# Optimization experiments

Measured on AMD Instinct MI355X. Metric: run time of the kernel, lower is better.

Reference implementation:

```python
import jax, jax.numpy as jnp
import numpy as np

B, L, H, HD, NK, NQ = 2, 1024, 2048, 64, 4, 32
NPREV = NQ - NK  # 28 KV heads gathered from previous layers


def _rotate_half(x):
    x1, x2 = jnp.split(x, 2, axis=-1)
    return jnp.concatenate((-x2, x1), axis=-1)


def _apply_rope(cos, sin, x):
    length = x.shape[-2]
    return x * cos[..., -length:, :] + _rotate_half(x) * sin[..., -length:, :]


def setup_inputs() -> dict:
    key = jax.random.key(0)
    ks = jax.random.split(key, 7)
    hidden_states = jax.random.normal(ks[0], (B, L, H), jnp.float32)
    prev_k = jax.random.normal(ks[1], (B, NPREV, L, HD), jnp.float32)
    prev_v = jax.random.normal(ks[2], (B, NPREV, L, HD), jnp.float32)
    s = 0.02
    Wq = jax.random.normal(ks[3], (NQ * HD, H), jnp.float32) * s
    Wk = jax.random.normal(ks[4], (NK * HD, H), jnp.float32) * s
    Wv = jax.random.normal(ks[5], (NK * HD, H), jnp.float32) * s
    Wo = jax.random.normal(ks[6], (H, NQ * HD), jnp.float32) * s
    # RoPE tables (duplicated-half layout matching rotate_half)
    inv_freq = 1.0 / (10000.0 ** (jnp.arange(0, HD, 2, dtype=jnp.float32) / HD))
    freqs = jnp.arange(L, dtype=jnp.float32)[:, None] * inv_freq[None, :]
    emb = jnp.concatenate((freqs, freqs), axis=-1)  # [L, HD]
    cos = jnp.cos(emb)[None, None]  # [1,1,L,HD]
    sin = jnp.sin(emb)[None, None]
    attention_mask = jnp.tril(jnp.ones((L, L), dtype=bool))[None, None]  # [1,1,L,L]
    return {"hidden_states": hidden_states, "prev_k": prev_k, "prev_v": prev_v,
            "Wq": Wq, "Wk": Wk, "Wv": Wv, "Wo": Wo,
            "cos": cos, "sin": sin, "attention_mask": attention_mask}


def reference(hidden_states, prev_k, prev_v, Wq, Wk, Wv, Wo, cos, sin, attention_mask):
    Bv, Lv, _ = hidden_states.shape
    # QKV projections (torch Linear: x @ W.T)
    q = (hidden_states @ Wq.T).reshape(Bv, Lv, NQ, HD).transpose(0, 2, 1, 3)  # [B,NQ,L,HD]
    k_new = (hidden_states @ Wk.T).reshape(Bv, Lv, NK, HD).transpose(0, 2, 1, 3)
    v_new = (hidden_states @ Wv.T).reshape(Bv, Lv, NK, HD).transpose(0, 2, 1, 3)
    # DeCAN cross-layer cache update: stack previous layers' KV heads + current
    k = jnp.concatenate((prev_k, k_new), axis=1)  # [B,NQ,L,HD]
    v = jnp.concatenate((prev_v, v_new), axis=1)
    # RoPE after cache gather (same positions for all stacked layers)
    q = _apply_rope(cos, sin, q)
    k = _apply_rope(cos, sin, k)
    # SDPA with additive log-mask (log(bool) == 0 / -inf; broadcast == repeat)
    add_mask = jnp.where(attention_mask, jnp.float32(0.0), jnp.float32(-1e30))
    scores = jnp.einsum('bhqd,bhkd->bhqk', q, k) * (HD ** -0.5) + add_mask
    attn = jax.nn.softmax(scores, axis=-1)
    out = jnp.einsum('bhqk,bhkd->bhqd', attn, v)  # [B,NQ,L,HD]
    out = out.transpose(0, 2, 1, 3).reshape(Bv, Lv, NQ * HD)
    return out @ Wo.T  # [B,L,H]
```

## Files before the change

kernel.cpp:

```cpp
#include <hip/hip_runtime.h>
#include <stdint.h>

#define L_SEQ 1024
#define NHEAD 32
#define NPREV 28
#define HDIM  64
#define HID   2048
#define NPROJ 2560

typedef __bf16 bf16_t;
typedef bf16_t bf16x8 __attribute__((ext_vector_type(8)));
typedef float  f32x4  __attribute__((ext_vector_type(4)));

__device__ __forceinline__ ushort f2bf(float x) {
    union { float f; uint32_t u; } v; v.f = x;
    uint32_t r = v.u + 0x7fffu + ((v.u >> 16) & 1u);
    return (ushort)(r >> 16);
}
__device__ __forceinline__ ushort f2bf_t(float x) {
    union { float f; uint32_t u; } v; v.f = x;
    return (ushort)(v.u >> 16);
}
__device__ __forceinline__ float bf2f(ushort u) {
    union { uint32_t u; float f; } v; v.u = ((uint32_t)u) << 16; return v.f;
}
__device__ __forceinline__ void cvt8(float* dst, uint4 u) {
    union { uint32_t u; float f; } t;
    t.u = u.x << 16;         dst[0] = t.f;
    t.u = u.x & 0xffff0000u; dst[1] = t.f;
    t.u = u.y << 16;         dst[2] = t.f;
    t.u = u.y & 0xffff0000u; dst[3] = t.f;
    t.u = u.z << 16;         dst[4] = t.f;
    t.u = u.z & 0xffff0000u; dst[5] = t.f;
    t.u = u.w << 16;         dst[6] = t.f;
    t.u = u.w & 0xffff0000u; dst[7] = t.f;
}

#define GLB(p) ((const __attribute__((address_space(1))) void*)(p))
#define LDS(p) ((__attribute__((address_space(3))) void*)(p))

__global__ void cvt_all(const float* __restrict__ s0, const float* __restrict__ s1,
                        const float* __restrict__ s2, const float* __restrict__ s3,
                        const float* __restrict__ s4,
                        ushort* __restrict__ d0, ushort* __restrict__ d1,
                        ushort* __restrict__ d2, ushort* __restrict__ d3,
                        ushort* __restrict__ d4) {
    int blk = blockIdx.x;
    const float* src; ushort* dst; int idx;
    if      (blk < 4096) { src = s0; dst = d0; idx = blk; }
    else if (blk < 8192) { src = s1; dst = d1; idx = blk - 4096; }
    else if (blk < 8704) { src = s2; dst = d2; idx = blk - 8192; }
    else if (blk < 9216) { src = s3; dst = d3; idx = blk - 8704; }
    else                 { src = s4; dst = d4; idx = blk - 9216; }
    int i = idx * 256 + threadIdx.x;
    float4 v = ((const float4*)src)[i];
    ushort4 o;
    o.x = f2bf(v.x); o.y = f2bf(v.y); o.z = f2bf(v.z); o.w = f2bf(v.w);
    ((ushort4*)dst)[i] = o;
}

__global__ __launch_bounds__(256, 3) void gemm1_fused(
        const ushort* __restrict__ A, const ushort* __restrict__ B,
        ushort* __restrict__ C0, ushort* __restrict__ C1,
        const float* __restrict__ prev_k, const float* __restrict__ prev_v,
        const float* __restrict__ cosb, const float* __restrict__ sinb,
        ushort* __restrict__ Kr, ushort* __restrict__ Vt) {
    __shared__ __align__(16) ushort Ash[2 * 4096];
    __shared__ __align__(16) ushort Bsh[2 * 8192];
    const int g   = blockIdx.x;
    const int tid = threadIdx.x;

    if (g < 1280) {
        const int K = 2048, N = NPROJ;
        const int lane = tid & 63;
        const int wave = tid >> 6;
        const int quad = lane >> 4;
        const int l16  = lane & 15;
        const int z  = g / 640;
        const int rb = g % 640;
        const int n0 = (rb % 20) * 128;
        const int m0 = (rb / 20) * 64;
        const int wm = (wave >> 1) * 32;
        const int wn = (wave & 1) * 64;
        const int kb = z * 1024;
        const int ke = kb + 1024;
        ushort* C = z ? C1 : C0;

        f32x4 acc[2][4] = {};

        const int sb = ((tid & 3) ^ ((tid >> 3) & 3)) * 8;
        const ushort* Ag = A + (long)(m0 + (tid >> 2)) * K + sb;
        const ushort* Bg = B + (long)(n0 + (tid >> 2)) * K + sb;
        const int woff = wave * 512;
        const int swz = (quad ^ ((l16 >> 1) & 3)) * 8;

        __builtin_amdgcn_global_load_lds(GLB(Ag + kb),                LDS(Ash + woff),               16, 0, 0);
        __builtin_amdgcn_global_load_lds(GLB(Ag + kb + 32),           LDS(Ash + 2048 + woff),        16, 0, 0);
        __builtin_amdgcn_global_load_lds(GLB(Bg + kb),                LDS(Bsh + woff),               16, 0, 0);
        __builtin_amdgcn_global_load_lds(GLB(Bg + 64L * K + kb),      LDS(Bsh + 2048 + woff),        16, 0, 0);
        __builtin_amdgcn_global_load_lds(GLB(Bg + kb + 32),           LDS(Bsh + 4096 + woff),        16, 0, 0);
        __builtin_amdgcn_global_load_lds(GLB(Bg + 64L * K + kb + 32), LDS(Bsh + 4096 + 2048 + woff), 16, 0, 0);

        int cur = 0;
        for (int k0 = kb; k0 < ke; k0 += 64) {
            __syncthreads();
            if (k0 + 64 < ke) {
                const int na = (cur ^ 1) * 4096;
                const int nb = (cur ^ 1) * 8192;
                const ushort* Agn = Ag + k0 + 64;
                const ushort* Bgn = Bg + k0 + 64;
                __builtin_amdgcn_global_load_lds(GLB(Agn),                LDS(Ash + na + woff),               16, 0, 0);
                __builtin_amdgcn_global_load_lds(GLB(Agn + 32),           LDS(Ash + na + 2048 + woff),        16, 0, 0);
                __builtin_amdgcn_global_load_lds(GLB(Bgn),                LDS(Bsh + nb + woff),               16, 0, 0);
                __builtin_amdgcn_global_load_lds(GLB(Bgn + 64L * K),      LDS(Bsh + nb + 2048 + woff),        16, 0, 0);
                __builtin_amdgcn_global_load_lds(GLB(Bgn + 32),           LDS(Bsh + nb + 4096 + woff),        16, 0, 0);
                __builtin_amdgcn_global_load_lds(GLB(Bgn + 64L * K + 32), LDS(Bsh + nb + 4096 + 2048 + woff), 16, 0, 0);
            }
            const ushort* As = Ash + cur * 4096;
            const ushort* Bs = Bsh + cur * 8192;
#pragma unroll
            for (int h = 0; h < 2; h++) {
                bf16x8 af[2], bf[4];
#pragma unroll
                for (int i = 0; i < 2; i++)
                    af[i] = *(const bf16x8*)(As + h * 2048 + (wm + i * 16 + l16) * 32 + swz);
#pragma unroll
                for (int i = 0; i < 4; i++)
                    bf[i] = *(const bf16x8*)(Bs + h * 4096 + (wn + i * 16 + l16) * 32 + swz);
#pragma unroll
                for (int mi = 0; mi < 2; mi++)
#pragma unroll
                    for (int ni = 0; ni < 4; ni++)
                        acc[mi][ni] = __builtin_amdgcn_mfma_f32_16x16x32_bf16(af[mi], bf[ni], acc[mi][ni], 0, 0, 0);
            }
            cur ^= 1;
        }
#pragma unroll
        for (int mi = 0; mi < 2; mi++)
#pragma unroll
            for (int ni = 0; ni < 4; ni++)
#pragma unroll
                for (int r = 0; r < 4; r++) {
                    int m = m0 + wm + mi * 16 + quad * 4 + r;
                    int n = n0 + wn + ni * 16 + l16;
                    C[(long)m * N + n] = f2bf(acc[mi][ni][r]);
                }
    } else {
        const int idx = g - 1280;
        const int lt  = idx & 15;
        const int ph  = idx >> 4;
        const int b   = ph / NPREV;
        const int h   = ph % NPREV;
        const int l0  = lt * 64;
        const int r   = tid >> 2;
        const int c0  = (tid & 3) * 8;
        const int l   = l0 + r;
        const int bh  = b * NHEAD + h;
        const long base = (long)bh * (L_SEQ * HDIM);

        float cv[8], sv[8];
        *(float4*)(cv)     = *(const float4*)(cosb + l * 64 + c0);
        *(float4*)(cv + 4) = *(const float4*)(cosb + l * 64 + c0 + 4);
        *(float4*)(sv)     = *(const float4*)(sinb + l * 64 + c0);
        *(float4*)(sv + 4) = *(const float4*)(sinb + l * 64 + c0 + 4);

        {
            const float* pk = prev_k + (((long)b * NPREV + h) * L_SEQ + l) * 64;
            float xl[8], xh[8];
            *(float4*)(xl)     = *(const float4*)(pk + c0);
            *(float4*)(xl + 4) = *(const float4*)(pk + c0 + 4);
            *(float4*)(xh)     = *(const float4*)(pk + c0 + 32);
            *(float4*)(xh + 4) = *(const float4*)(pk + c0 + 36);
            ushort ol[8], oh[8];
#pragma unroll
            for (int i = 0; i < 8; i++) {
                ol[i] = f2bf(xl[i] * cv[i] - xh[i] * sv[i]);
                oh[i] = f2bf(xh[i] * cv[i] + xl[i] * sv[i]);
            }
            ushort* k = Kr + base + (long)l * 64;
            *(uint4*)(k + c0)      = *(uint4*)ol;
            *(uint4*)(k + c0 + 32) = *(uint4*)oh;
        }
        {
            ushort* T = Ash;
            const float* pv = prev_v + (((long)b * NPREV + h) * L_SEQ + l) * 64;
            float xl[8], xh[8];
            *(float4*)(xl)     = *(const float4*)(pv + c0);
            *(float4*)(xl + 4) = *(const float4*)(pv + c0 + 4);
            *(float4*)(xh)     = *(const float4*)(pv + c0 + 32);
            *(float4*)(xh + 4) = *(const float4*)(pv + c0 + 36);
#pragma unroll
            for (int i = 0; i < 8; i++) {
                T[(c0 + i) * 72 + r]      = f2bf(xl[i]);
                T[(c0 + 32 + i) * 72 + r] = f2bf(xh[i]);
            }
            __syncthreads();
            const int lc = (tid & 3) * 16;
            uint4 o0 = *(const uint4*)(T + r * 72 + lc);
            uint4 o1 = *(const uint4*)(T + r * 72 + lc + 8);
            ushort* og = Vt + base + (long)r * L_SEQ + l0 + lc;
            *(uint4*)og       = o0;
            *(uint4*)(og + 8) = o1;
        }
    }
}

__global__ __launch_bounds__(256) void prep_new(const ushort* __restrict__ pa,
                                                const ushort* __restrict__ pb,
                                                const float* __restrict__ cosb,
                                                const float* __restrict__ sinb,
                                                ushort* __restrict__ Qr,
                                                ushort* __restrict__ Kr,
                                                ushort* __restrict__ Vt) {
    __shared__ __align__(16) ushort T[64 * 72];
    const int t  = threadIdx.x;
    const int l0 = blockIdx.x * 64;
    const int bh = blockIdx.y;
    const int b  = bh >> 5, h = bh & 31;
    const int r  = t >> 2;
    const int c0 = (t & 3) * 8;
    const int l  = l0 + r;
    const long prow = ((long)(b * L_SEQ + l)) * NPROJ;
    const long base = (long)bh * (L_SEQ * HDIM);

    float cv[8], sv[8];
    *(float4*)(cv)     = *(const float4*)(cosb + l * 64 + c0);
    *(float4*)(cv + 4) = *(const float4*)(cosb + l * 64 + c0 + 4);
    *(float4*)(sv)     = *(const float4*)(sinb + l * 64 + c0);
    *(float4*)(sv + 4) = *(const float4*)(sinb + l * 64 + c0 + 4);

    const float SC = 0.125f * 1.44269504f;

    {
        float xl[8], xh[8], yl[8], yh[8];
        cvt8(xl, *(const uint4*)(pa + prow + h * 64 + c0));
        cvt8(xh, *(const uint4*)(pa + prow + h * 64 + c0 + 32));
        cvt8(yl, *(const uint4*)(pb + prow + h * 64 + c0));
        cvt8(yh, *(const uint4*)(pb + prow + h * 64 + c0 + 32));
        ushort ol[8], oh[8];
#pragma unroll
        for (int i = 0; i < 8; i++) {
            float a = xl[i] + yl[i], c = xh[i] + yh[i];
            ol[i] = f2bf((a * cv[i] - c * sv[i]) * SC);
            oh[i] = f2bf((c * cv[i] + a * sv[i]) * SC);
        }
        ushort* q = Qr + base + (long)l * 64;
        *(uint4*)(q + c0)      = *(uint4*)ol;
        *(uint4*)(q + c0 + 32) = *(uint4*)oh;
    }
    if (h < NPREV) return;

    {
        float xl[8], xh[8], yl[8], yh[8];
        cvt8(xl, *(const uint4*)(pa + prow + HID + (h - NPREV) * 64 + c0));
        cvt8(xh, *(const uint4*)(pa + prow + HID + (h - NPREV) * 64 + c0 + 32));
        cvt8(yl, *(const uint4*)(pb + prow + HID + (h - NPREV) * 64 + c0));
        cvt8(yh, *(const uint4*)(pb + prow + HID + (h - NPREV) * 64 + c0 + 32));
        ushort ol[8], oh[8];
#pragma unroll
        for (int i = 0; i < 8; i++) {
            float a = xl[i] + yl[i], c = xh[i] + yh[i];
            ol[i] = f2bf(a * cv[i] - c * sv[i]);
            oh[i] = f2bf(c * cv[i] + a * sv[i]);
        }
        ushort* k = Kr + base + (long)l * 64;
        *(uint4*)(k + c0)      = *(uint4*)ol;
        *(uint4*)(k + c0 + 32) = *(uint4*)oh;
    }
    {
        float xl[8], xh[8], yl[8], yh[8];
        cvt8(xl, *(const uint4*)(pa + prow + HID + 256 + (h - NPREV) * 64 + c0));
        cvt8(xh, *(const uint4*)(pa + prow + HID + 256 + (h - NPREV) * 64 + c0 + 32));
        cvt8(yl, *(const uint4*)(pb + prow + HID + 256 + (h - NPREV) * 64 + c0));
        cvt8(yh, *(const uint4*)(pb + prow + HID + 256 + (h - NPREV) * 64 + c0 + 32));
#pragma unroll
        for (int i = 0; i < 8; i++) {
            T[(c0 + i) * 72 + r]      = f2bf(xl[i] + yl[i]);
            T[(c0 + 32 + i) * 72 + r] = f2bf(xh[i] + yh[i]);
        }
        __syncthreads();
        const int lc = (t & 3) * 16;
        uint4 o0 = *(const uint4*)(T + r * 72 + lc);
        uint4 o1 = *(const uint4*)(T + r * 72 + lc + 8);
        ushort* og = Vt + base + (long)r * L_SEQ + l0 + lc;
        *(uint4*)og       = o0;
        *(uint4*)(og + 8) = o1;
    }
}

#define KP 68
__global__ __launch_bounds__(256, 4) void attn_mfma(const ushort* __restrict__ Qr,
                                                    const ushort* __restrict__ Kr,
                                                    const ushort* __restrict__ Vt,
                                                    ushort* __restrict__ Oa) {
    __shared__ __align__(16) ushort Ksh[64 * KP];
    __shared__ __align__(16) ushort Vsh[64 * KP];
    __shared__ __align__(16) ushort Psh[4][16 * KP];

    const int tid  = threadIdx.x;
    const int lane = tid & 63;
    const int wave = tid >> 6;
    const int quad = lane >> 4;
    const int l16  = lane & 15;
    const int bh   = blockIdx.x;
    const int q0   = (15 - (int)blockIdx.y) * 64;
    const long base = (long)bh * (L_SEQ * HDIM);

    bf16x8 qf0, qf1;
    {
        const ushort* qp = Qr + base + (long)(q0 + wave * 16 + l16) * HDIM + quad * 8;
        qf0 = *(const bf16x8*)qp;
        qf1 = *(const bf16x8*)(qp + 32);
    }
    float lr[4] = {};
    f32x4 o[4] = {};

    const int srow  = tid >> 2;
    const int scol  = (tid & 3) * 16;
    const int row_l = wave * 16 + quad * 4;

    uint4 ka, kb, va, vb;
    {
        const ushort* kg = Kr + base + (long)srow * HDIM + scol;
        ka = *(const uint4*)kg; kb = *(const uint4*)(kg + 8);
        const ushort* vg = Vt + base + (long)srow * L_SEQ + scol;
        va = *(const uint4*)vg; vb = *(const uint4*)(vg + 8);
    }

    for (int kv0 = 0; kv0 <= q0; kv0 += 64) {
        __syncthreads();
        *(uint4*)(Ksh + srow * KP + scol)     = ka;
        *(uint4*)(Ksh + srow * KP + scol + 8) = kb;
        *(uint4*)(Vsh + srow * KP + scol)     = va;
        *(uint4*)(Vsh + srow * KP + scol + 8) = vb;
        __syncthreads();
        if (kv0 + 64 <= q0) {
            const ushort* kg = Kr + base + (long)(kv0 + 64 + srow) * HDIM + scol;
            ka = *(const uint4*)kg; kb = *(const uint4*)(kg + 8);
            const ushort* vg = Vt + base + (long)srow * L_SEQ + kv0 + 64 + scol;
            va = *(const uint4*)vg; vb = *(const uint4*)(vg + 8);
        }

        f32x4 s[4] = {};
#pragma unroll
        for (int nt = 0; nt < 4; nt++) {
            bf16x8 kf0 = *(const bf16x8*)(Ksh + (nt * 16 + l16) * KP + quad * 8);
            bf16x8 kf1 = *(const bf16x8*)(Ksh + (nt * 16 + l16) * KP + 32 + quad * 8);
            s[nt] = __builtin_amdgcn_mfma_f32_16x16x32_bf16(qf0, kf0, s[nt], 0, 0, 0);
            s[nt] = __builtin_amdgcn_mfma_f32_16x16x32_bf16(qf1, kf1, s[nt], 0, 0, 0);
        }

        const bool diag = (kv0 == q0);
#pragma unroll
        for (int nt = 0; nt < 4; nt++) {
            const int col = nt * 16 + l16;
#pragma unroll
            for (int r = 0; r < 4; r++) {
                float p = __builtin_exp2f(s[nt][r]);
                if (diag && col > row_l + r) p = 0.f;
                lr[r] += p;
                Psh[wave][(quad * 4 + r) * KP + col] = f2bf_t(p);
            }
        }

#pragma unroll
        for (int ks = 0; ks < 2; ks++) {
            bf16x8 pf = *(const bf16x8*)(&Psh[wave][l16 * KP + ks * 32 + quad * 8]);
#pragma unroll
            for (int nt = 0; nt < 4; nt++) {
                bf16x8 vf = *(const bf16x8*)(Vsh + (nt * 16 + l16) * KP + ks * 32 + quad * 8);
                o[nt] = __builtin_amdgcn_mfma_f32_16x16x32_bf16(pf, vf, o[nt], 0, 0, 0);
            }
        }
    }

    const int b = bh >> 5, h = bh & 31;
#pragma unroll
    for (int r = 0; r < 4; r++) {
        float a = lr[r];
        a += __shfl_xor(a, 1); a += __shfl_xor(a, 2); a += __shfl_xor(a, 4); a += __shfl_xor(a, 8);
        float inv = 1.f / a;
        long orow = (long)(b * L_SEQ + q0 + wave * 16 + quad * 4 + r) * HID + h * 64;
#pragma unroll
        for (int nt = 0; nt < 4; nt++)
            Oa[orow + nt * 16 + l16] = f2bf(o[nt][r] * inv);
    }
}

__global__ __launch_bounds__(256, 3) void gemm_out(const ushort* __restrict__ A,
                                                   const ushort* __restrict__ B,
                                                   float* __restrict__ C) {
    __shared__ __align__(16) ushort Ash[2 * 4096];
    __shared__ __align__(16) ushort Bsh[2 * 8192];
    const int K = 2048, N = 2048;
    const int tid  = threadIdx.x;
    const int lane = tid & 63;
    const int wave = tid >> 6;
    const int quad = lane >> 4;
    const int l16  = lane & 15;
    const int m0 = blockIdx.y * 64;
    const int n0 = blockIdx.x * 128;
    const int wm = (wave >> 1) * 32;
    const int wn = (wave & 1) * 64;

    f32x4 acc[2][4] = {};

    const int sb = ((tid & 3) ^ ((tid >> 3) & 3)) * 8;
    const ushort* Ag = A + (long)(m0 + (tid >> 2)) * K + sb;
    const ushort* Bg = B + (long)(n0 + (tid >> 2)) * K + sb;
    const int woff = wave * 512;
    const int swz = (quad ^ ((l16 >> 1) & 3)) * 8;

    __builtin_amdgcn_global_load_lds(GLB(Ag),                LDS(Ash + woff),               16, 0, 0);
    __builtin_amdgcn_global_load_lds(GLB(Ag + 32),           LDS(Ash + 2048 + woff),        16, 0, 0);
    __builtin_amdgcn_global_load_lds(GLB(Bg),                LDS(Bsh + woff),               16, 0, 0);
    __builtin_amdgcn_global_load_lds(GLB(Bg + 64L * K),      LDS(Bsh + 2048 + woff),        16, 0, 0);
    __builtin_amdgcn_global_load_lds(GLB(Bg + 32),           LDS(Bsh + 4096 + woff),        16, 0, 0);
    __builtin_amdgcn_global_load_lds(GLB(Bg + 64L * K + 32), LDS(Bsh + 4096 + 2048 + woff), 16, 0, 0);

    int cur = 0;
    for (int k0 = 0; k0 < K; k0 += 64) {
        __syncthreads();
        if (k0 + 64 < K) {
            const int na = (cur ^ 1) * 4096;
            const int nb = (cur ^ 1) * 8192;
            const ushort* Agn = Ag + k0 + 64;
            const ushort* Bgn = Bg + k0 + 64;
            __builtin_amdgcn_global_load_lds(GLB(Agn),                LDS(Ash + na + woff),               16, 0, 0);
            __builtin_amdgcn_global_load_lds(GLB(Agn + 32),           LDS(Ash + na + 2048 + woff),        16, 0, 0);
            __builtin_amdgcn_global_load_lds(GLB(Bgn),                LDS(Bsh + nb + woff),               16, 0, 0);
            __builtin_amdgcn_global_load_lds(GLB(Bgn + 64L * K),      LDS(Bsh + nb + 2048 + woff),        16, 0, 0);
            __builtin_amdgcn_global_load_lds(GLB(Bgn + 32),           LDS(Bsh + nb + 4096 + woff),        16, 0, 0);
            __builtin_amdgcn_global_load_lds(GLB(Bgn + 64L * K + 32), LDS(Bsh + nb + 4096 + 2048 + woff), 16, 0, 0);
        }
        const ushort* As = Ash + cur * 4096;
        const ushort* Bs = Bsh + cur * 8192;
#pragma unroll
        for (int h = 0; h < 2; h++) {
            bf16x8 af[2], bf[4];
#pragma unroll
            for (int i = 0; i < 2; i++)
                af[i] = *(const bf16x8*)(As + h * 2048 + (wm + i * 16 + l16) * 32 + swz);
#pragma unroll
            for (int i = 0; i < 4; i++)
                bf[i] = *(const bf16x8*)(Bs + h * 4096 + (wn + i * 16 + l16) * 32 + swz);
#pragma unroll
            for (int mi = 0; mi < 2; mi++)
#pragma unroll
                for (int ni = 0; ni < 4; ni++)
                    acc[mi][ni] = __builtin_amdgcn_mfma_f32_16x16x32_bf16(af[mi], bf[ni], acc[mi][ni], 0, 0, 0);
        }
        cur ^= 1;
    }
#pragma unroll
    for (int mi = 0; mi < 2; mi++)
#pragma unroll
        for (int ni = 0; ni < 4; ni++)
#pragma unroll
            for (int r = 0; r < 4; r++) {
                int m = m0 + wm + mi * 16 + quad * 4 + r;
                int n = n0 + wn + ni * 16 + l16;
                C[(long)m * N + n] = acc[mi][ni][r];
            }
}

extern "C" void kernel_launch(void* const* d_in, const int* in_sizes, int n_in,
                              void* d_out, int out_size, void* d_ws, size_t ws_size,
                              hipStream_t stream) {
    const float* hs     = (const float*)d_in[0];
    const float* prev_k = (const float*)d_in[1];
    const float* prev_v = (const float*)d_in[2];
    const float* Wq     = (const float*)d_in[3];
    const float* Wk     = (const float*)d_in[4];
    const float* Wv     = (const float*)d_in[5];
    const float* Wo     = (const float*)d_in[6];
    const float* cosb   = (const float*)d_in[7];
    const float* sinb   = (const float*)d_in[8];
    float* out = (float*)d_out;

    ushort* hs_bf   = (ushort*)d_ws;
    ushort* wqkv_bf = hs_bf + 2048L * 2048;
    ushort* wo_bf   = wqkv_bf + 2560L * 2048;
    ushort* proj    = wo_bf + 2048L * 2048;
    ushort* Qr      = proj + 2048L * 2560;
    ushort* Kr      = Qr + 4194304;
    ushort* Vt      = Kr + 4194304;
    ushort* Oa      = Vt + 4194304;

    ushort* proj_b;
    if (ws_size >= (35651584UL + 5242880UL) * 2)
        proj_b = Oa + 4194304;
    else
        proj_b = (ushort*)(void*)d_in[0];

    cvt_all<<<13312, 256, 0, stream>>>(hs, Wq, Wk, Wv, Wo,
                                       hs_bf, wqkv_bf,
                                       wqkv_bf + 2048L * 2048,
                                       wqkv_bf + 2304L * 2048,
                                       wo_bf);
    gemm1_fused<<<2176, 256, 0, stream>>>(hs_bf, wqkv_bf, proj, proj_b,
                                          prev_k, prev_v, cosb, sinb, Kr, Vt);
    prep_new<<<dim3(16, 64), 256, 0, stream>>>(proj, proj_b, cosb, sinb, Qr, Kr, Vt);
    attn_mfma<<<dim3(64, 16), 256, 0, stream>>>(Qr, Kr, Vt, Oa);
    gemm_out<<<dim3(16, 32), 256, 0, stream>>>(Oa, wo_bf, out);
}
```

Measured before the change: 233.0 us.

## Fuse RoPE, scaling and Q/K/V scatter into QKV GEMM epilogue, drop split-K

The QKV projection GEMM now runs the full K=2048 reduction per block instead of a two-way split-K, and its epilogue applies RoPE and the softmax scale directly, writing Q, K and transposed V into their attention layouts. This removes the intermediate projection buffers, the partial-sum add, and the separate prep_new kernel launch with its extra global round trip. In exchange there are half as many GEMM blocks, each with a longer K loop, and the epilogue does scattered 2-byte stores (especially the strided transposed V writes) instead of coalesced row stores.

Measured after the change: 224.3 us. -3.7%, faster.

```diff
diff --git a/kernel.cpp b/kernel.cpp
--- a/kernel.cpp
+++ b/kernel.cpp
@@ -61,30 +61,24 @@
 
 __global__ __launch_bounds__(256, 3) void gemm1_fused(
         const ushort* __restrict__ A, const ushort* __restrict__ B,
-        ushort* __restrict__ C0, ushort* __restrict__ C1,
         const float* __restrict__ prev_k, const float* __restrict__ prev_v,
         const float* __restrict__ cosb, const float* __restrict__ sinb,
-        ushort* __restrict__ Kr, ushort* __restrict__ Vt) {
+        ushort* __restrict__ Qr, ushort* __restrict__ Kr, ushort* __restrict__ Vt) {
     __shared__ __align__(16) ushort Ash[2 * 4096];
     __shared__ __align__(16) ushort Bsh[2 * 8192];
     const int g   = blockIdx.x;
     const int tid = threadIdx.x;
 
-    if (g < 1280) {
-        const int K = 2048, N = NPROJ;
+    if (g < 640) {
+        const int K = 2048;
         const int lane = tid & 63;
         const int wave = tid >> 6;
         const int quad = lane >> 4;
         const int l16  = lane & 15;
-        const int z  = g / 640;
-        const int rb = g % 640;
-        const int n0 = (rb % 20) * 128;
-        const int m0 = (rb / 20) * 64;
+        const int n0 = (g % 20) * 128;
+        const int m0 = (g / 20) * 64;
         const int wm = (wave >> 1) * 32;
         const int wn = (wave & 1) * 64;
-        const int kb = z * 1024;
-        const int ke = kb + 1024;
-        ushort* C = z ? C1 : C0;
 
         f32x4 acc[2][4] = {};
 
@@ -94,17 +88,17 @@
         const int woff = wave * 512;
         const int swz = (quad ^ ((l16 >> 1) & 3)) * 8;
 
-        __builtin_amdgcn_global_load_lds(GLB(Ag + kb),                LDS(Ash + woff),               16, 0, 0);
-        __builtin_amdgcn_global_load_lds(GLB(Ag + kb + 32),           LDS(Ash + 2048 + woff),        16, 0, 0);
-        __builtin_amdgcn_global_load_lds(GLB(Bg + kb),                LDS(Bsh + woff),               16, 0, 0);
-        __builtin_amdgcn_global_load_lds(GLB(Bg + 64L * K + kb),      LDS(Bsh + 2048 + woff),        16, 0, 0);
-        __builtin_amdgcn_global_load_lds(GLB(Bg + kb + 32),           LDS(Bsh + 4096 + woff),        16, 0, 0);
-        __builtin_amdgcn_global_load_lds(GLB(Bg + 64L * K + kb + 32), LDS(Bsh + 4096 + 2048 + woff), 16, 0, 0);
+        __builtin_amdgcn_global_load_lds(GLB(Ag),                LDS(Ash + woff),               16, 0, 0);
+        __builtin_amdgcn_global_load_lds(GLB(Ag + 32),           LDS(Ash + 2048 + woff),        16, 0, 0);
+        __builtin_amdgcn_global_load_lds(GLB(Bg),                LDS(Bsh + woff),               16, 0, 0);
+        __builtin_amdgcn_global_load_lds(GLB(Bg + 64L * K),      LDS(Bsh + 2048 + woff),        16, 0, 0);
+        __builtin_amdgcn_global_load_lds(GLB(Bg + 32),           LDS(Bsh + 4096 + woff),        16, 0, 0);
+        __builtin_amdgcn_global_load_lds(GLB(Bg + 64L * K + 32), LDS(Bsh + 4096 + 2048 + woff), 16, 0, 0);
 
         int cur = 0;
-        for (int k0 = kb; k0 < ke; k0 += 64) {
+        for (int k0 = 0; k0 < K; k0 += 64) {
             __syncthreads();
-            if (k0 + 64 < ke) {
+            if (k0 + 64 < K) {
                 const int na = (cur ^ 1) * 4096;
                 const int nb = (cur ^ 1) * 8192;
                 const ushort* Agn = Ag + k0 + 64;
@@ -135,18 +129,65 @@
             }
             cur ^= 1;
         }
-#pragma unroll
-        for (int mi = 0; mi < 2; mi++)
-#pragma unroll
-            for (int ni = 0; ni < 4; ni++)
+
+        const int colbase = n0 + wn;
+        const int b  = (m0 + wm) >> 10;
+        const float SC = 0.125f * 1.44269504f;
+
+        if (colbase < HID) {
+            const int h  = colbase >> 6;
+            const long qb = ((long)(b * NHEAD + h)) * (L_SEQ * HDIM);
+#pragma unroll
+            for (int mi = 0; mi < 2; mi++)
 #pragma unroll
                 for (int r = 0; r < 4; r++) {
-                    int m = m0 + wm + mi * 16 + quad * 4 + r;
-                    int n = n0 + wn + ni * 16 + l16;
-                    C[(long)m * N + n] = f2bf(acc[mi][ni][r]);
+                    const int m = m0 + wm + mi * 16 + quad * 4 + r;
+                    const int l = m & 1023;
+                    const float c0v = cosb[l * 64 + l16];
+                    const float c1v = cosb[l * 64 + 16 + l16];
+                    const float s0v = sinb[l * 64 + l16];
+                    const float s1v = sinb[l * 64 + 16 + l16];
+                    ushort* q = Qr + qb + (long)l * 64;
+                    q[l16]      = f2bf((acc[mi][0][r] * c0v - acc[mi][2][r] * s0v) * SC);
+                    q[16 + l16] = f2bf((acc[mi][1][r] * c1v - acc[mi][3][r] * s1v) * SC);
+                    q[32 + l16] = f2bf((acc[mi][2][r] * c0v + acc[mi][0][r] * s0v) * SC);
+                    q[48 + l16] = f2bf((acc[mi][3][r] * c1v + acc[mi][1][r] * s1v) * SC);
                 }
+        } else if (colbase < HID + 256) {
+            const int h  = NPREV + ((colbase - HID) >> 6);
+            const long kb2 = ((long)(b * NHEAD + h)) * (L_SEQ * HDIM);
+#pragma unroll
+            for (int mi = 0; mi < 2; mi++)
+#pragma unroll
+                for (int r = 0; r < 4; r++) {
+                    const int m = m0 + wm + mi * 16 + quad * 4 + r;
+                    const int l = m & 1023;
+                    const float c0v = cosb[l * 64 + l16];
+                    const float c1v = cosb[l * 64 + 16 + l16];
+                    const float s0v = sinb[l * 64 + l16];
+                    const float s1v = sinb[l * 64 + 16 + l16];
+                    ushort* k = Kr + kb2 + (long)l * 64;
+                    k[l16]      = f2bf(acc[mi][0][r] * c0v - acc[mi][2][r] * s0v);
+                    k[16 + l16] = f2bf(acc[mi][1][r] * c1v - acc[mi][3][r] * s1v);
+                    k[32 + l16] = f2bf(acc[mi][2][r] * c0v + acc[mi][0][r] * s0v);
+                    k[48 + l16] = f2bf(acc[mi][3][r] * c1v + acc[mi][1][r] * s1v);
+                }
+        } else {
+            const int h  = NPREV + ((colbase - HID - 256) >> 6);
+            const long vb = ((long)(b * NHEAD + h)) * (L_SEQ * HDIM);
+#pragma unroll
+            for (int mi = 0; mi < 2; mi++)
+#pragma unroll
+                for (int r = 0; r < 4; r++) {
+                    const int m = m0 + wm + mi * 16 + quad * 4 + r;
+                    const int l = m & 1023;
+#pragma unroll
+                    for (int nt = 0; nt < 4; nt++)
+                        Vt[vb + (long)(nt * 16 + l16) * L_SEQ + l] = f2bf(acc[mi][nt][r]);
+                }
+        }
     } else {
-        const int idx = g - 1280;
+        const int idx = g - 640;
         const int lt  = idx & 15;
         const int ph  = idx >> 4;
         const int b   = ph / NPREV;
@@ -202,89 +243,6 @@
             *(uint4*)og       = o0;
             *(uint4*)(og + 8) = o1;
         }
-    }
-}
-
-__global__ __launch_bounds__(256) void prep_new(const ushort* __restrict__ pa,
-                                                const ushort* __restrict__ pb,
-                                                const float* __restrict__ cosb,
-                                                const float* __restrict__ sinb,
-                                                ushort* __restrict__ Qr,
-                                                ushort* __restrict__ Kr,
-                                                ushort* __restrict__ Vt) {
-    __shared__ __align__(16) ushort T[64 * 72];
-    const int t  = threadIdx.x;
-    const int l0 = blockIdx.x * 64;
-    const int bh = blockIdx.y;
-    const int b  = bh >> 5, h = bh & 31;
-    const int r  = t >> 2;
-    const int c0 = (t & 3) * 8;
-    const int l  = l0 + r;
-    const long prow = ((long)(b * L_SEQ + l)) * NPROJ;
-    const long base = (long)bh * (L_SEQ * HDIM);
-
-    float cv[8], sv[8];
-    *(float4*)(cv)     = *(const float4*)(cosb + l * 64 + c0);
-    *(float4*)(cv + 4) = *(const float4*)(cosb + l * 64 + c0 + 4);
-    *(float4*)(sv)     = *(const float4*)(sinb + l * 64 + c0);
-    *(float4*)(sv + 4) = *(const float4*)(sinb + l * 64 + c0 + 4);
-
-    const float SC = 0.125f * 1.44269504f;
-
-    {
-        float xl[8], xh[8], yl[8], yh[8];
-        cvt8(xl, *(const uint4*)(pa + prow + h * 64 + c0));
-        cvt8(xh, *(const uint4*)(pa + prow + h * 64 + c0 + 32));
-        cvt8(yl, *(const uint4*)(pb + prow + h * 64 + c0));
-        cvt8(yh, *(const uint4*)(pb + prow + h * 64 + c0 + 32));
-        ushort ol[8], oh[8];
-#pragma unroll
-        for (int i = 0; i < 8; i++) {
-            float a = xl[i] + yl[i], c = xh[i] + yh[i];
-            ol[i] = f2bf((a * cv[i] - c * sv[i]) * SC);
-            oh[i] = f2bf((c * cv[i] + a * sv[i]) * SC);
-        }
-        ushort* q = Qr + base + (long)l * 64;
-        *(uint4*)(q + c0)      = *(uint4*)ol;
-        *(uint4*)(q + c0 + 32) = *(uint4*)oh;
-    }
-    if (h < NPREV) return;
-
-    {
-        float xl[8], xh[8], yl[8], yh[8];
-        cvt8(xl, *(const uint4*)(pa + prow + HID + (h - NPREV) * 64 + c0));
-        cvt8(xh, *(const uint4*)(pa + prow + HID + (h - NPREV) * 64 + c0 + 32));
-        cvt8(yl, *(const uint4*)(pb + prow + HID + (h - NPREV) * 64 + c0));
-        cvt8(yh, *(const uint4*)(pb + prow + HID + (h - NPREV) * 64 + c0 + 32));
-        ushort ol[8], oh[8];
-#pragma unroll
-        for (int i = 0; i < 8; i++) {
-            float a = xl[i] + yl[i], c = xh[i] + yh[i];
-            ol[i] = f2bf(a * cv[i] - c * sv[i]);
-            oh[i] = f2bf(c * cv[i] + a * sv[i]);
-        }
-        ushort* k = Kr + base + (long)l * 64;
-        *(uint4*)(k + c0)      = *(uint4*)ol;
-        *(uint4*)(k + c0 + 32) = *(uint4*)oh;
-    }
-    {
-        float xl[8], xh[8], yl[8], yh[8];
-        cvt8(xl, *(const uint4*)(pa + prow + HID + 256 + (h - NPREV) * 64 + c0));
-        cvt8(xh, *(const uint4*)(pa + prow + HID + 256 + (h - NPREV) * 64 + c0 + 32));
-        cvt8(yl, *(const uint4*)(pb + prow + HID + 256 + (h - NPREV) * 64 + c0));
-        cvt8(yh, *(const uint4*)(pb + prow + HID + 256 + (h - NPREV) * 64 + c0 + 32));
-#pragma unroll
-        for (int i = 0; i < 8; i++) {
-            T[(c0 + i) * 72 + r]      = f2bf(xl[i] + yl[i]);
-            T[(c0 + 32 + i) * 72 + r] = f2bf(xh[i] + yh[i]);
-        }
-        __syncthreads();
-        const int lc = (t & 3) * 16;
-        uint4 o0 = *(const uint4*)(T + r * 72 + lc);
-        uint4 o1 = *(const uint4*)(T + r * 72 + lc + 8);
-        ushort* og = Vt + base + (long)r * L_SEQ + l0 + lc;
-        *(uint4*)og       = o0;
-        *(uint4*)(og + 8) = o1;
     }
 }
 
@@ -481,26 +439,18 @@
     ushort* hs_bf   = (ushort*)d_ws;
     ushort* wqkv_bf = hs_bf + 2048L * 2048;
     ushort* wo_bf   = wqkv_bf + 2560L * 2048;
-    ushort* proj    = wo_bf + 2048L * 2048;
-    ushort* Qr      = proj + 2048L * 2560;
+    ushort* Qr      = wo_bf + 2048L * 2048;
     ushort* Kr      = Qr + 4194304;
     ushort* Vt      = Kr + 4194304;
     ushort* Oa      = Vt + 4194304;
-
-    ushort* proj_b;
-    if (ws_size >= (35651584UL + 5242880UL) * 2)
-        proj_b = Oa + 4194304;
-    else
-        proj_b = (ushort*)(void*)d_in[0];
 
     cvt_all<<<13312, 256, 0, stream>>>(hs, Wq, Wk, Wv, Wo,
                                        hs_bf, wqkv_bf,
                                        wqkv_bf + 2048L * 2048,
                                        wqkv_bf + 2304L * 2048,
                                        wo_bf);
-    gemm1_fused<<<2176, 256, 0, stream>>>(hs_bf, wqkv_bf, proj, proj_b,
-                                          prev_k, prev_v, cosb, sinb, Kr, Vt);
-    prep_new<<<dim3(16, 64), 256, 0, stream>>>(proj, proj_b, cosb, sinb, Qr, Kr, Vt);
+    gemm1_fused<<<1536, 256, 0, stream>>>(hs_bf, wqkv_bf,
+                                          prev_k, prev_v, cosb, sinb, Qr, Kr, Vt);
     attn_mfma<<<dim3(64, 16), 256, 0, stream>>>(Qr, Kr, Vt, Oa);
     gemm_out<<<dim3(16, 32), 256, 0, stream>>>(Oa, wo_bf, out);
 }
```
